# Optimization experiments

Measured on AMD Instinct MI355X. Metric: run time of the kernel, lower is better.

Reference implementation:

```python
import jax, jax.numpy as jnp
import numpy as np

B, NX, NY, C, H = 4, 1024, 1024, 768, 12
D = C // H  # head dim = 64
LN_EPS = 1e-5


def _dwconv(x_bcn, w, b, pad):
    # depthwise 1D conv: x [B,C,N], w [C,1,K], groups=C
    out = jax.lax.conv_general_dilated(
        x_bcn, w, window_strides=(1,), padding=[(pad, pad)],
        dimension_numbers=("NCH", "OIH", "NCH"), feature_group_count=C)
    return out + b[None, :, None]


def setup_inputs() -> dict:
    key = jax.random.key(0)
    ks = jax.random.split(key, 16)
    s = 0.02
    inp = {
        "x": jax.random.normal(ks[0], (B, NX, C), jnp.float32),
        "y": jax.random.normal(ks[1], (B, NY, C), jnp.float32),
        "conv1_w": jax.random.normal(ks[2], (C, 1, 3), jnp.float32) * s,
        "conv1_b": jnp.zeros((C,), jnp.float32),
        "conv2_w": jax.random.normal(ks[3], (C, 1, 5), jnp.float32) * s,
        "conv2_b": jnp.zeros((C,), jnp.float32),
        "conv3_w": jax.random.normal(ks[4], (C, 1, 7), jnp.float32) * s,
        "conv3_b": jnp.zeros((C,), jnp.float32),
        "ln_w": jnp.ones((C,), jnp.float32),
        "ln_b": jnp.zeros((C,), jnp.float32),
        "q_w": jax.random.normal(ks[5], (C, C), jnp.float32) * s,
        "kv_w": jax.random.normal(ks[6], (2 * C, C), jnp.float32) * s,
        "proj_w": jax.random.normal(ks[7], (C, C), jnp.float32) * s,
        "proj_b": jnp.zeros((C,), jnp.float32),
        "k1": int(NY * (1.0 / (1.0 + np.exp(-0.5)))),   # 637, from sigmoid(k_ratio1=0.5)
        "k2": int(NY * (1.0 / (1.0 + np.exp(-0.25)))),  # 575, from sigmoid(k_ratio2=0.25)
    }
    return inp


def reference(x, y, conv1_w, conv1_b, conv2_w, conv2_b, conv3_w, conv3_b,
              ln_w, ln_b, q_w, kv_w, proj_w, proj_b, k1, k2):
    yp = jnp.swapaxes(y, 1, 2)  # [B,C,Ny]
    # multi-scale depthwise convs; stride=1, same-padding -> all outputs length Ny,
    # so the original F.interpolate(size=target_len) is an exact identity.
    y_sum = _dwconv(yp, conv1_w, conv1_b, 1) + _dwconv(yp, conv2_w, conv2_b, 2) \
          + _dwconv(yp, conv3_w, conv3_b, 3)
    y_sum = jnp.swapaxes(y_sum, 1, 2)  # [B,Ny,C]
    # LayerNorm
    mu = y_sum.mean(-1, keepdims=True)
    var = ((y_sum - mu) ** 2).mean(-1, keepdims=True)
    y_norm = (y_sum - mu) * jax.lax.rsqrt(var + LN_EPS) * ln_w + ln_b
    # kv projection -> k,v [B,H,Ny,D]
    kv = (y_norm @ kv_w.T).reshape(B, NY, 2, H, D).transpose(2, 0, 3, 1, 4)
    k, v = kv[0], kv[1]
    q = (x @ q_w.T).reshape(B, NX, H, D).transpose(0, 2, 1, 3)  # [B,H,Nx,D]
    scale = D ** -0.5
    attn = jnp.einsum("bhqd,bhkd->bhqk", q, k) * scale  # [B,H,Nx,Ny]

    def topk_softmax(a, kk):
        # keep top-kk scores per row, mask rest to -inf, softmax
        kth = jax.lax.top_k(a, kk)[0][..., -1:]
        a_masked = jnp.where(a >= kth, a, -jnp.inf)
        return jax.nn.softmax(a_masked, axis=-1)

    out1 = jnp.einsum("bhqk,bhkd->bhqd", topk_softmax(attn, k1), v)
    out2 = jnp.einsum("bhqk,bhkd->bhqd", topk_softmax(attn, k2), v)
    out = 0.6 * out1 + 0.4 * out2
    out = out.transpose(0, 2, 1, 3).reshape(B, NX, C)
    out = out @ proj_w.T + proj_b
    return out + x
```

## Files before the change

### kernel.cpp

```cpp
#include <hip/hip_runtime.h>
#include <stdint.h>

#define B_ 4
#define NX_ 1024
#define NY_ 1024
#define C_ 768
#define H_ 12

using bf16x8 = __attribute__((ext_vector_type(8))) short;
using f32x4  = __attribute__((ext_vector_type(4))) float;

__device__ __forceinline__ unsigned short f2bf(float f) {
  union { float f; uint32_t u; } v; v.f = f;
  return (unsigned short)((v.u + 0x7FFFu + ((v.u >> 16) & 1u)) >> 16);
}
__device__ __forceinline__ float bf2f(uint32_t h) {
  union { uint32_t u; float f; } v; v.u = h << 16;
  return v.f;
}
__device__ __forceinline__ uint32_t umaxu(uint32_t a, uint32_t b) { return a > b ? a : b; }
__device__ __forceinline__ uint32_t uminu(uint32_t a, uint32_t b) { return a < b ? a : b; }
__device__ __forceinline__ uint32_t rfl(uint32_t v) {
  return (uint32_t)__builtin_amdgcn_readfirstlane((int)v);
}
__device__ __forceinline__ uint32_t key2h(uint32_t k) {
  return k ^ ((k & 0x8000u) ? 0x8000u : 0xFFFFu);
}
__device__ __forceinline__ float key2f(uint32_t k) { return bf2f(key2h(k)); }
__device__ __forceinline__ uint32_t f2key(float f) {
  const uint32_t h = f2bf(f);
  return h ^ (0x8000u | (0xFFFFu * (h >> 15)));
}

__global__ __launch_bounds__(256) void pre_kernel(
    const float* __restrict__ y,
    const float* __restrict__ w1, const float* __restrict__ b1,
    const float* __restrict__ w2, const float* __restrict__ b2,
    const float* __restrict__ w3, const float* __restrict__ b3,
    const float* __restrict__ lnw, const float* __restrict__ lnb,
    unsigned short* __restrict__ ynorm,
    const float4* __restrict__ x, uint2* __restrict__ xo,
    const float4* __restrict__ qw, uint2* __restrict__ qo,
    const float4* __restrict__ kvw, uint2* __restrict__ kvo,
    const float4* __restrict__ pw, uint2* __restrict__ po) {
  __shared__ float red[4][8];
  const int bid = blockIdx.x;
  const int t = threadIdx.x;
  if (bid >= 1024) {
    const int cid = bid - 1024;
    const float4* s; uint2* d; int base; float sc = 1.0f;
    if (cid < 3072)      { s = x;   d = xo;  base = cid;        sc = 0.125f * 1.44269504f; }
    else if (cid < 3648) { s = qw;  d = qo;  base = cid - 3072; }
    else if (cid < 4800) { s = kvw; d = kvo; base = cid - 3648; }
    else                 { s = pw;  d = po;  base = cid - 4800; }
    const int i = base * 256 + t;
    float4 v = s[i];
    uint2 p;
    p.x = (uint32_t)f2bf(v.x * sc) | ((uint32_t)f2bf(v.y * sc) << 16);
    p.y = (uint32_t)f2bf(v.z * sc) | ((uint32_t)f2bf(v.w * sc) << 16);
    d[i] = p;
    return;
  }
  const int b = bid >> 8, n0 = (bid & 255) << 2;
  const float* yb = y + (size_t)b * NY_ * C_;
  float v[3][4];
  #pragma unroll
  for (int ci = 0; ci < 3; ci++) {
    const int c = t + (ci << 8);
    float co[7];
    #pragma unroll
    for (int k = 0; k < 7; k++) co[k] = w3[c * 7 + k];
    #pragma unroll
    for (int k = 0; k < 5; k++) co[k + 1] += w2[c * 5 + k];
    #pragma unroll
    for (int k = 0; k < 3; k++) co[k + 2] += w1[c * 3 + k];
    const float bias = b1[c] + b2[c] + b3[c];
    float rv[10];
    #pragma unroll
    for (int rr = 0; rr < 10; rr++) {
      const int nn = n0 - 3 + rr;
      rv[rr] = (nn >= 0 && nn < NY_) ? yb[(size_t)nn * C_ + c] : 0.0f;
    }
    #pragma unroll
    for (int oi = 0; oi < 4; oi++) {
      float acc = bias;
      #pragma unroll
      for (int k = 0; k < 7; k++) acc = fmaf(co[k], rv[oi + k], acc);
      v[ci][oi] = acc;
    }
  }
  float s4[4], q4[4];
  #pragma unroll
  for (int oi = 0; oi < 4; oi++) {
    s4[oi] = v[0][oi] + v[1][oi] + v[2][oi];
    q4[oi] = v[0][oi] * v[0][oi] + v[1][oi] * v[1][oi] + v[2][oi] * v[2][oi];
  }
  #pragma unroll
  for (int m = 32; m >= 1; m >>= 1) {
    #pragma unroll
    for (int oi = 0; oi < 4; oi++) {
      s4[oi] += __shfl_xor(s4[oi], m);
      q4[oi] += __shfl_xor(q4[oi], m);
    }
  }
  const int wid = t >> 6;
  if ((t & 63) == 0) {
    #pragma unroll
    for (int oi = 0; oi < 4; oi++) { red[wid][oi] = s4[oi]; red[wid][4 + oi] = q4[oi]; }
  }
  __syncthreads();
  const float inv = 1.0f / 768.0f;
  #pragma unroll
  for (int oi = 0; oi < 4; oi++) {
    const float ts = red[0][oi] + red[1][oi] + red[2][oi] + red[3][oi];
    const float tq = red[0][4 + oi] + red[1][4 + oi] + red[2][4 + oi] + red[3][4 + oi];
    const float mu = ts * inv;
    const float var = tq * inv - mu * mu;
    const float rs = rsqrtf(var + 1e-5f);
    unsigned short* op = ynorm + (size_t)(b * 1024 + n0 + oi) * C_;
    #pragma unroll
    for (int ci = 0; ci < 3; ci++) {
      const int c = t + (ci << 8);
      op[c] = f2bf((v[ci][oi] - mu) * rs * lnw[c] + lnb[c]);
    }
  }
}

template <int ROWS>
__device__ __forceinline__ void stage_tile(const unsigned short* __restrict__ src,
                                           unsigned short* lds, int tid) {
  #pragma unroll
  for (int c = 0; c < ROWS / 32; c++) {
    const int lin = c * 4096 + (tid >> 6) * 1024 + (tid & 63) * 16;
    const int r = lin >> 7;
    const int koff = (lin & 127) ^ ((r & 7) << 4);
    const char* g = (const char*)(src + (size_t)r * 768) + koff;
    __builtin_amdgcn_global_load_lds(
        (const __attribute__((address_space(1))) uint32_t*)g,
        (__attribute__((address_space(3))) uint32_t*)(lds + (c * 2048 + (tid >> 6) * 512)),
        16, 0, 0);
  }
}

__device__ __forceinline__ void gemm_core(const unsigned short* __restrict__ A,
                                          const unsigned short* __restrict__ BT,
                                          int m0, int n0,
                                          unsigned short* Alds, unsigned short* Blds,
                                          f32x4 (&acc)[4][2]) {
  const int tid = threadIdx.x;
  const int l = tid & 63, w = tid >> 6;
  const int lr = l & 15, lk = l >> 4;
  const int wm = (w >> 1) * 64, wn = (w & 1) * 32;
  #pragma unroll
  for (int i = 0; i < 4; i++)
    #pragma unroll
    for (int j = 0; j < 2; j++) acc[i][j] = (f32x4){0.f, 0.f, 0.f, 0.f};

  for (int kt = 0; kt < 768; kt += 64) {
    __syncthreads();
    stage_tile<128>(A + (size_t)m0 * 768 + kt, Alds, tid);
    stage_tile<64>(BT + (size_t)n0 * 768 + kt, Blds, tid);
    asm volatile("s_waitcnt vmcnt(0)" ::: "memory");
    __syncthreads();
    #pragma unroll
    for (int s = 0; s < 2; s++) {
      bf16x8 a[4], b[2];
      #pragma unroll
      for (int i = 0; i < 4; i++) {
        const int r = wm + i * 16 + lr;
        const int byte = r * 128 + ((s * 64 + lk * 16) ^ ((r & 7) << 4));
        a[i] = *(const bf16x8*)((const char*)Alds + byte);
      }
      #pragma unroll
      for (int j = 0; j < 2; j++) {
        const int r = wn + j * 16 + lr;
        const int byte = r * 128 + ((s * 64 + lk * 16) ^ ((r & 7) << 4));
        b[j] = *(const bf16x8*)((const char*)Blds + byte);
      }
      #pragma unroll
      for (int i = 0; i < 4; i++)
        #pragma unroll
        for (int j = 0; j < 2; j++)
          acc[i][j] = __builtin_amdgcn_mfma_f32_16x16x32_bf16(a[i], b[j], acc[i][j], 0, 0, 0);
    }
  }
}

__global__ __launch_bounds__(256) void gemm_qkv_kernel(
    const unsigned short* __restrict__ xbf, const unsigned short* __restrict__ ynorm,
    const unsigned short* __restrict__ qwbf, const unsigned short* __restrict__ kvwbf,
    unsigned short* __restrict__ qbuf, unsigned short* __restrict__ kbuf,
    unsigned short* __restrict__ vtbuf) {
  __shared__ unsigned short Alds[128 * 64];
  __shared__ unsigned short Blds[64 * 64];
  const int bx = blockIdx.x;
  const bool isQ = bx < 12;
  const unsigned short* A = isQ ? xbf : ynorm;
  const unsigned short* BT = isQ ? qwbf : kvwbf;
  const int n0 = (isQ ? bx : bx - 12) * 64;
  const int m0 = blockIdx.y * 128;
  f32x4 acc[4][2];
  gemm_core(A, BT, m0, n0, Alds, Blds, acc);

  const int l = threadIdx.x & 63, w = threadIdx.x >> 6;
  const int lr = l & 15, lk = l >> 4;
  const int wm = (w >> 1) * 64, wn = (w & 1) * 32;
  #pragma unroll
  for (int i = 0; i < 4; i++) {
    const int r0 = m0 + wm + i * 16 + lk * 4;
    #pragma unroll
    for (int j = 0; j < 2; j++) {
      const int c = n0 + wn + j * 16 + lr;
      if (isQ) {
        const int h = c >> 6, d = c & 63;
        #pragma unroll
        for (int g = 0; g < 4; g++) {
          const int row = r0 + g;
          const int bb = row >> 10, nn = row & 1023;
          qbuf[((((size_t)bb * H_ + h) << 10) + nn) * 64 + d] = f2bf(acc[i][j][g]);
        }
      } else if (c < C_) {
        const int h = c >> 6, d = c & 63;
        #pragma unroll
        for (int g = 0; g < 4; g++) {
          const int row = r0 + g;
          const int bb = row >> 10, nn = row & 1023;
          kbuf[((((size_t)bb * H_ + h) << 10) + nn) * 64 + d] = f2bf(acc[i][j][g]);
        }
      } else {
        const int c2 = c - C_;
        const int h = c2 >> 6, d = c2 & 63;
        const int bb = r0 >> 10, nn = r0 & 1023;
        uint2 p;
        p.x = (uint32_t)f2bf(acc[i][j][0]) | ((uint32_t)f2bf(acc[i][j][1]) << 16);
        p.y = (uint32_t)f2bf(acc[i][j][2]) | ((uint32_t)f2bf(acc[i][j][3]) << 16);
        *(uint2*)(vtbuf + (((size_t)bb * H_ + h) * 64 + d) * 1024 + nn) = p;
      }
    }
  }
}

__global__ __launch_bounds__(256) void gemm_proj_kernel(
    const unsigned short* __restrict__ A, const unsigned short* __restrict__ BT,
    float* __restrict__ out, const float* __restrict__ bias,
    const float* __restrict__ resid) {
  __shared__ unsigned short Alds[128 * 64];
  __shared__ unsigned short Blds[64 * 64];
  const int n0 = blockIdx.x * 64;
  const int m0 = blockIdx.y * 128;
  f32x4 acc[4][2];
  gemm_core(A, BT, m0, n0, Alds, Blds, acc);

  const int l = threadIdx.x & 63, w = threadIdx.x >> 6;
  const int lr = l & 15, lk = l >> 4;
  const int wm = (w >> 1) * 64, wn = (w & 1) * 32;
  #pragma unroll
  for (int i = 0; i < 4; i++) {
    const int r0 = m0 + wm + i * 16 + lk * 4;
    #pragma unroll
    for (int j = 0; j < 2; j++) {
      const int c = n0 + wn + j * 16 + lr;
      #pragma unroll
      for (int g = 0; g < 4; g++) {
        const size_t idx = (size_t)(r0 + g) * C_ + c;
        out[idx] = acc[i][j][g] + bias[c] + resid[idx];
      }
    }
  }
}

struct SR { uint32_t t; uint32_t c; };
__device__ __forceinline__ SR searchk(const uint32_t (&k)[16], uint32_t kn,
                                      uint32_t lo, uint32_t clo, float flo,
                                      uint32_t hi, float fhi) {
  uint32_t chi = 0;
  #pragma unroll 1
  for (int it = 0; it < 16; ++it) {
    const int active = (clo > kn + 8u) && (lo + 1u < hi);
    if (!__builtin_amdgcn_readfirstlane(active)) break;
    uint32_t tk;
    if (it & 1) {
      tk = (lo + hi) >> 1;
    } else {
      const float tf = flo + (fhi - flo) * (float)(clo - kn) / (float)(clo - chi);
      tk = f2key(tf);
    }
    tk = uminu(umaxu(tk, lo + 1u), hi - 1u);
    uint32_t cnt = 0;
    #pragma unroll
    for (int i = 0; i < 16; i++) cnt += (k[i] >= tk) ? 1u : 0u;
    #pragma unroll
    for (int m = 32; m >= 1; m >>= 1) cnt += (uint32_t)__shfl_xor((int)cnt, m);
    const float tfk = key2f(tk);
    if (cnt >= kn) { lo = tk; clo = cnt; flo = tfk; }
    else           { hi = tk; chi = cnt; fhi = tfk; }
  }
  return {lo, clo};
}

__global__ __launch_bounds__(512, 8) void attn_kernel(
    const unsigned short* __restrict__ qbuf,
    const unsigned short* __restrict__ kbuf,
    const unsigned short* __restrict__ vtbuf,
    unsigned short* __restrict__ ao,
    const int* __restrict__ k1p, const int* __restrict__ k2p) {
  __shared__ unsigned short W[16 * 1024];
  __shared__ float P[16 * 66];
  const int l = threadIdx.x & 63, w = threadIdx.x >> 6;
  const int lr = l & 15, lk = l >> 4;
  const int bh = blockIdx.y, qt = blockIdx.x;
  const uint32_t kn1 = rfl(k1p[0]), kn2 = rfl(k2p[0]);
  const size_t base = (size_t)bh * NY_ * 64;
  const unsigned short* Q = qbuf + base + (size_t)qt * 16 * 64;
  const unsigned short* Kp = kbuf + base;
  const unsigned short* Vt = vtbuf + base;

  bf16x8 qf[2];
  #pragma unroll
  for (int s = 0; s < 2; s++)
    qf[s] = *(const bf16x8*)(Q + lr * 64 + s * 32 + lk * 8);

  #pragma unroll
  for (int kc = 0; kc < 2; kc++) {
    const int kbase = w * 128 + kc * 64;
    f32x4 acc[4];
    #pragma unroll
    for (int i = 0; i < 4; i++) acc[i] = (f32x4){0.f, 0.f, 0.f, 0.f};
    #pragma unroll
    for (int s = 0; s < 2; s++) {
      bf16x8 kf[4];
      #pragma unroll
      for (int i = 0; i < 4; i++)
        kf[i] = *(const bf16x8*)(Kp + (size_t)(kbase + i * 16 + lr) * 64 + s * 32 + lk * 8);
      #pragma unroll
      for (int i = 0; i < 4; i++)
        acc[i] = __builtin_amdgcn_mfma_f32_16x16x32_bf16(kf[i], qf[s], acc[i], 0, 0, 0);
    }
    #pragma unroll
    for (int i = 0; i < 4; i++) {
      const int kk = kbase + i * 16 + lk * 4;
      uint2 p;
      p.x = (uint32_t)f2bf(acc[i][0]) | ((uint32_t)f2bf(acc[i][1]) << 16);
      p.y = (uint32_t)f2bf(acc[i][2]) | ((uint32_t)f2bf(acc[i][3]) << 16);
      const int byte = lr * 2048 + ((kk * 2) ^ ((lr & 7) << 4));
      *(uint2*)((char*)W + byte) = p;
    }
  }
  __syncthreads();

  #pragma unroll 1
  for (int rr = 0; rr < 2; rr++) {
    char* rp = (char*)W + (2 * w + rr) * 2048;
    const uint4 u0 = *(uint4*)(rp + 16 * l);
    const uint4 u1 = *(uint4*)(rp + 16 * l + 1024);
    uint32_t k[16];
    {
      const uint32_t uu[8] = {u0.x, u0.y, u0.z, u0.w, u1.x, u1.y, u1.z, u1.w};
      #pragma unroll
      for (int i = 0; i < 8; i++) {
        const uint32_t h0 = uu[i] & 0xFFFFu, h1 = uu[i] >> 16;
        k[2 * i]     = h0 ^ (0x8000u | (0xFFFFu * (h0 >> 15)));
        k[2 * i + 1] = h1 ^ (0x8000u | (0xFFFFu * (h1 >> 15)));
      }
    }
    uint32_t kmx = 0;
    #pragma unroll
    for (int i = 0; i < 16; i++) kmx = umaxu(kmx, k[i]);
    #pragma unroll
    for (int m = 32; m >= 1; m >>= 1)
      kmx = umaxu(kmx, (uint32_t)__shfl_xor((int)kmx, m));
    const float fmx = key2f(kmx);

    const SR r1 = searchk(k, kn1, 0u, 1024u, fmx - 12.0f, kmx + 1u, fmx);
    const SR r2 = searchk(k, kn2, r1.t, r1.c, key2f(r1.t), kmx + 1u, fmx);
    const uint32_t t1 = r1.t, t2 = r2.t;

    float top = 0.f, band = 0.f;
    #pragma unroll
    for (int i = 0; i < 16; i++) {
      const float e = exp2f(key2f(k[i]) - fmx);
      if (k[i] >= t2) top += e;
      else if (k[i] >= t1) band += e;
    }
    #pragma unroll
    for (int m = 32; m >= 1; m >>= 1) {
      top += __shfl_xor(top, m);
      band += __shfl_xor(band, m);
    }
    const float c1 = 0.6f / (top + band), c2 = 0.4f / top;
    const float c12 = c1 + c2;
    uint32_t o[8];
    #pragma unroll
    for (int i = 0; i < 8; i++) {
      const int i0 = 2 * i, i1 = 2 * i + 1;
      const float cf0 = (k[i0] >= t1) ? ((k[i0] >= t2) ? c12 : c1) : 0.f;
      const float cf1 = (k[i1] >= t1) ? ((k[i1] >= t2) ? c12 : c1) : 0.f;
      const float w0 = exp2f(key2f(k[i0]) - fmx) * cf0;
      const float w1 = exp2f(key2f(k[i1]) - fmx) * cf1;
      o[i] = (uint32_t)f2bf(w0) | ((uint32_t)f2bf(w1) << 16);
    }
    *(uint4*)(rp + 16 * l)        = (uint4){o[0], o[1], o[2], o[3]};
    *(uint4*)(rp + 16 * l + 1024) = (uint4){o[4], o[5], o[6], o[7]};
  }
  __syncthreads();

  const int d0 = (w & 3) * 16;
  const int k0 = (w >> 2) * 512;
  f32x4 oacc = (f32x4){0.f, 0.f, 0.f, 0.f};
  #pragma unroll 4
  for (int kt2 = 0; kt2 < 512; kt2 += 32) {
    const int kt = k0 + kt2;
    const bf16x8 vf = *(const bf16x8*)(Vt + (size_t)(d0 + lr) * 1024 + kt + lk * 8);
    const int byte = lr * 2048 + (((kt + lk * 8) * 2) ^ ((lr & 7) << 4));
    const bf16x8 wf = *(const bf16x8*)((char*)W + byte);
    oacc = __builtin_amdgcn_mfma_f32_16x16x32_bf16(wf, vf, oacc, 0, 0, 0);
  }
  if (w >= 4) {
    #pragma unroll
    for (int g = 0; g < 4; g++)
      P[(lk * 4 + g) * 66 + d0 + lr] = oacc[g];
  }
  __syncthreads();
  if (w < 4) {
    const int b = bh / H_, h = bh % H_;
    #pragma unroll
    for (int g = 0; g < 4; g++) {
      const float v = oacc[g] + P[(lk * 4 + g) * 66 + d0 + lr];
      const int qrow = qt * 16 + lk * 4 + g;
      ao[(size_t)(b * NX_ + qrow) * C_ + h * 64 + d0 + lr] = f2bf(v);
    }
  }
}

extern "C" void kernel_launch(void* const* d_in, const int* in_sizes, int n_in,
                              void* d_out, int out_size, void* d_ws, size_t ws_size,
                              hipStream_t stream) {
  const float* x   = (const float*)d_in[0];
  const float* y   = (const float*)d_in[1];
  const float* w1  = (const float*)d_in[2];
  const float* b1  = (const float*)d_in[3];
  const float* w2  = (const float*)d_in[4];
  const float* b2  = (const float*)d_in[5];
  const float* w3  = (const float*)d_in[6];
  const float* b3  = (const float*)d_in[7];
  const float* lnw = (const float*)d_in[8];
  const float* lnb = (const float*)d_in[9];
  const float* qw  = (const float*)d_in[10];
  const float* kvw = (const float*)d_in[11];
  const float* pw  = (const float*)d_in[12];
  const float* pb  = (const float*)d_in[13];
  const int* k1p   = (const int*)d_in[14];
  const int* k2p   = (const int*)d_in[15];

  char* ws = (char*)d_ws;
  size_t off = 0;
  auto alloc = [&](size_t bytes) {
    char* p = ws + off;
    off += (bytes + 255) & ~(size_t)255;
    return p;
  };
  const size_t NTOK = (size_t)B_ * NX_ * C_;
  unsigned short* x_bf   = (unsigned short*)alloc(NTOK * 2);
  unsigned short* ynorm  = (unsigned short*)alloc(NTOK * 2);
  unsigned short* qw_bf  = (unsigned short*)alloc((size_t)C_ * C_ * 2);
  unsigned short* kvw_bf = (unsigned short*)alloc((size_t)2 * C_ * C_ * 2);
  unsigned short* pw_bf  = (unsigned short*)alloc((size_t)C_ * C_ * 2);
  unsigned short* qbuf   = (unsigned short*)alloc(NTOK * 2);
  unsigned short* kbuf   = (unsigned short*)alloc(NTOK * 2);
  unsigned short* vtbuf  = (unsigned short*)alloc(NTOK * 2);
  unsigned short* aobuf  = (unsigned short*)alloc(NTOK * 2);

  pre_kernel<<<6400, 256, 0, stream>>>(
      y, w1, b1, w2, b2, w3, b3, lnw, lnb, ynorm,
      (const float4*)x, (uint2*)x_bf, (const float4*)qw, (uint2*)qw_bf,
      (const float4*)kvw, (uint2*)kvw_bf, (const float4*)pw, (uint2*)pw_bf);

  gemm_qkv_kernel<<<dim3(36, 32), 256, 0, stream>>>(
      x_bf, ynorm, qw_bf, kvw_bf, qbuf, kbuf, vtbuf);

  attn_kernel<<<dim3(NX_ / 16, B_ * H_), 512, 0, stream>>>(qbuf, kbuf, vtbuf, aobuf, k1p, k2p);

  gemm_proj_kernel<<<dim3(12, 32), 256, 0, stream>>>(
      aobuf, pw_bf, (float*)d_out, pb, x);
}
```

Before: 295.1 us.

## Widen GEMM tiles to 128x128 and switch top-k threshold search to float domain

The GEMM core now computes 128x128 output tiles per block, with each wave owning a 64x64 sub-tile, instead of 128x64. This halves the grid for the QKV and projection GEMMs and improves operand reuse per LDS stage, at the cost of more accumulator registers and fewer blocks in flight. The attention top-k threshold search now runs on float scores rather than order-preserving integer keys. It starts from a Gaussian quantile guess built from the row mean and variance, alternates interpolation with bisection, and stops once the bracket is narrower than 1e-3. The attention kernel's occupancy hint drops from 8 to 6, and the early exit could let the chosen threshold differ slightly from the exact k-th value.

```diff
diff --git a/kernel.cpp b/kernel.cpp
--- a/kernel.cpp
+++ b/kernel.cpp
@@ -14,22 +14,8 @@
   union { float f; uint32_t u; } v; v.f = f;
   return (unsigned short)((v.u + 0x7FFFu + ((v.u >> 16) & 1u)) >> 16);
 }
-__device__ __forceinline__ float bf2f(uint32_t h) {
-  union { uint32_t u; float f; } v; v.u = h << 16;
-  return v.f;
-}
-__device__ __forceinline__ uint32_t umaxu(uint32_t a, uint32_t b) { return a > b ? a : b; }
-__device__ __forceinline__ uint32_t uminu(uint32_t a, uint32_t b) { return a < b ? a : b; }
 __device__ __forceinline__ uint32_t rfl(uint32_t v) {
   return (uint32_t)__builtin_amdgcn_readfirstlane((int)v);
-}
-__device__ __forceinline__ uint32_t key2h(uint32_t k) {
-  return k ^ ((k & 0x8000u) ? 0x8000u : 0xFFFFu);
-}
-__device__ __forceinline__ float key2f(uint32_t k) { return bf2f(key2h(k)); }
-__device__ __forceinline__ uint32_t f2key(float f) {
-  const uint32_t h = f2bf(f);
-  return h ^ (0x8000u | (0xFFFFu * (h >> 15)));
 }
 
 __global__ __launch_bounds__(256) void pre_kernel(
@@ -142,45 +128,45 @@
   }
 }
 
-__device__ __forceinline__ void gemm_core(const unsigned short* __restrict__ A,
-                                          const unsigned short* __restrict__ BT,
-                                          int m0, int n0,
-                                          unsigned short* Alds, unsigned short* Blds,
-                                          f32x4 (&acc)[4][2]) {
+__device__ __forceinline__ void gemm_core128(const unsigned short* __restrict__ A,
+                                             const unsigned short* __restrict__ BT,
+                                             int m0, int n0,
+                                             unsigned short* Alds, unsigned short* Blds,
+                                             f32x4 (&acc)[4][4]) {
   const int tid = threadIdx.x;
   const int l = tid & 63, w = tid >> 6;
   const int lr = l & 15, lk = l >> 4;
-  const int wm = (w >> 1) * 64, wn = (w & 1) * 32;
+  const int wr = (w >> 1) * 64, wc = (w & 1) * 64;
   #pragma unroll
   for (int i = 0; i < 4; i++)
     #pragma unroll
-    for (int j = 0; j < 2; j++) acc[i][j] = (f32x4){0.f, 0.f, 0.f, 0.f};
+    for (int j = 0; j < 4; j++) acc[i][j] = (f32x4){0.f, 0.f, 0.f, 0.f};
 
   for (int kt = 0; kt < 768; kt += 64) {
     __syncthreads();
     stage_tile<128>(A + (size_t)m0 * 768 + kt, Alds, tid);
-    stage_tile<64>(BT + (size_t)n0 * 768 + kt, Blds, tid);
+    stage_tile<128>(BT + (size_t)n0 * 768 + kt, Blds, tid);
     asm volatile("s_waitcnt vmcnt(0)" ::: "memory");
     __syncthreads();
     #pragma unroll
     for (int s = 0; s < 2; s++) {
-      bf16x8 a[4], b[2];
+      bf16x8 a[4], b[4];
       #pragma unroll
       for (int i = 0; i < 4; i++) {
-        const int r = wm + i * 16 + lr;
+        const int r = wr + i * 16 + lr;
         const int byte = r * 128 + ((s * 64 + lk * 16) ^ ((r & 7) << 4));
         a[i] = *(const bf16x8*)((const char*)Alds + byte);
       }
       #pragma unroll
-      for (int j = 0; j < 2; j++) {
-        const int r = wn + j * 16 + lr;
+      for (int j = 0; j < 4; j++) {
+        const int r = wc + j * 16 + lr;
         const int byte = r * 128 + ((s * 64 + lk * 16) ^ ((r & 7) << 4));
         b[j] = *(const bf16x8*)((const char*)Blds + byte);
       }
       #pragma unroll
       for (int i = 0; i < 4; i++)
         #pragma unroll
-        for (int j = 0; j < 2; j++)
+        for (int j = 0; j < 4; j++)
           acc[i][j] = __builtin_amdgcn_mfma_f32_16x16x32_bf16(a[i], b[j], acc[i][j], 0, 0, 0);
     }
   }
@@ -192,25 +178,25 @@
     unsigned short* __restrict__ qbuf, unsigned short* __restrict__ kbuf,
     unsigned short* __restrict__ vtbuf) {
   __shared__ unsigned short Alds[128 * 64];
-  __shared__ unsigned short Blds[64 * 64];
+  __shared__ unsigned short Blds[128 * 64];
   const int bx = blockIdx.x;
-  const bool isQ = bx < 12;
+  const bool isQ = bx < 6;
   const unsigned short* A = isQ ? xbf : ynorm;
   const unsigned short* BT = isQ ? qwbf : kvwbf;
-  const int n0 = (isQ ? bx : bx - 12) * 64;
+  const int n0 = (isQ ? bx : bx - 6) * 128;
   const int m0 = blockIdx.y * 128;
-  f32x4 acc[4][2];
-  gemm_core(A, BT, m0, n0, Alds, Blds, acc);
+  f32x4 acc[4][4];
+  gemm_core128(A, BT, m0, n0, Alds, Blds, acc);
 
   const int l = threadIdx.x & 63, w = threadIdx.x >> 6;
   const int lr = l & 15, lk = l >> 4;
-  const int wm = (w >> 1) * 64, wn = (w & 1) * 32;
+  const int wr = (w >> 1) * 64, wc = (w & 1) * 64;
   #pragma unroll
   for (int i = 0; i < 4; i++) {
-    const int r0 = m0 + wm + i * 16 + lk * 4;
-    #pragma unroll
-    for (int j = 0; j < 2; j++) {
-      const int c = n0 + wn + j * 16 + lr;
+    const int r0 = m0 + wr + i * 16 + lk * 4;
+    #pragma unroll
+    for (int j = 0; j < 4; j++) {
+      const int c = n0 + wc + j * 16 + lr;
       if (isQ) {
         const int h = c >> 6, d = c & 63;
         #pragma unroll
@@ -245,21 +231,21 @@
     float* __restrict__ out, const float* __restrict__ bias,
     const float* __restrict__ resid) {
   __shared__ unsigned short Alds[128 * 64];
-  __shared__ unsigned short Blds[64 * 64];
-  const int n0 = blockIdx.x * 64;
+  __shared__ unsigned short Blds[128 * 64];
+  const int n0 = blockIdx.x * 128;
   const int m0 = blockIdx.y * 128;
-  f32x4 acc[4][2];
-  gemm_core(A, BT, m0, n0, Alds, Blds, acc);
+  f32x4 acc[4][4];
+  gemm_core128(A, BT, m0, n0, Alds, Blds, acc);
 
   const int l = threadIdx.x & 63, w = threadIdx.x >> 6;
   const int lr = l & 15, lk = l >> 4;
-  const int wm = (w >> 1) * 64, wn = (w & 1) * 32;
+  const int wr = (w >> 1) * 64, wc = (w & 1) * 64;
   #pragma unroll
   for (int i = 0; i < 4; i++) {
-    const int r0 = m0 + wm + i * 16 + lk * 4;
-    #pragma unroll
-    for (int j = 0; j < 2; j++) {
-      const int c = n0 + wn + j * 16 + lr;
+    const int r0 = m0 + wr + i * 16 + lk * 4;
+    #pragma unroll
+    for (int j = 0; j < 4; j++) {
+      const int c = n0 + wc + j * 16 + lr;
       #pragma unroll
       for (int g = 0; g < 4; g++) {
         const size_t idx = (size_t)(r0 + g) * C_ + c;
@@ -269,36 +255,31 @@
   }
 }
 
-struct SR { uint32_t t; uint32_t c; };
-__device__ __forceinline__ SR searchk(const uint32_t (&k)[16], uint32_t kn,
-                                      uint32_t lo, uint32_t clo, float flo,
-                                      uint32_t hi, float fhi) {
-  uint32_t chi = 0;
+struct SRf { float t; uint32_t c; };
+__device__ __forceinline__ SRf searchf(const float (&s)[16], uint32_t kn,
+                                       float flo, uint32_t clo,
+                                       float fhi, uint32_t chi, float guess) {
+  float tf = guess;
   #pragma unroll 1
-  for (int it = 0; it < 16; ++it) {
-    const int active = (clo > kn + 8u) && (lo + 1u < hi);
-    if (!__builtin_amdgcn_readfirstlane(active)) break;
-    uint32_t tk;
-    if (it & 1) {
-      tk = (lo + hi) >> 1;
-    } else {
-      const float tf = flo + (fhi - flo) * (float)(clo - kn) / (float)(clo - chi);
-      tk = f2key(tf);
-    }
-    tk = uminu(umaxu(tk, lo + 1u), hi - 1u);
+  for (int it = 0; it < 12; ++it) {
+    if (!__builtin_amdgcn_readfirstlane((int)(clo > kn + 8u))) break;
+    if (!(tf > flo && tf < fhi)) tf = 0.5f * (flo + fhi);
     uint32_t cnt = 0;
     #pragma unroll
-    for (int i = 0; i < 16; i++) cnt += (k[i] >= tk) ? 1u : 0u;
+    for (int i = 0; i < 16; i++) cnt += (s[i] >= tf) ? 1u : 0u;
     #pragma unroll
     for (int m = 32; m >= 1; m >>= 1) cnt += (uint32_t)__shfl_xor((int)cnt, m);
-    const float tfk = key2f(tk);
-    if (cnt >= kn) { lo = tk; clo = cnt; flo = tfk; }
-    else           { hi = tk; chi = cnt; fhi = tfk; }
-  }
-  return {lo, clo};
-}
-
-__global__ __launch_bounds__(512, 8) void attn_kernel(
+    if (cnt >= kn) { flo = tf; clo = cnt; }
+    else           { fhi = tf; chi = cnt; }
+    if (fhi - flo < 1e-3f) break;
+    tf = (it & 1) ? 0.5f * (flo + fhi)
+                  : flo + (fhi - flo) * (float)(int)(clo - kn) /
+                        fmaxf((float)(int)(clo - chi), 1.0f);
+  }
+  return {flo, clo};
+}
+
+__global__ __launch_bounds__(512, 6) void attn_kernel(
     const unsigned short* __restrict__ qbuf,
     const unsigned short* __restrict__ kbuf,
     const unsigned short* __restrict__ vtbuf,
@@ -353,50 +334,59 @@
     char* rp = (char*)W + (2 * w + rr) * 2048;
     const uint4 u0 = *(uint4*)(rp + 16 * l);
     const uint4 u1 = *(uint4*)(rp + 16 * l + 1024);
-    uint32_t k[16];
+    float s[16];
     {
       const uint32_t uu[8] = {u0.x, u0.y, u0.z, u0.w, u1.x, u1.y, u1.z, u1.w};
       #pragma unroll
       for (int i = 0; i < 8; i++) {
-        const uint32_t h0 = uu[i] & 0xFFFFu, h1 = uu[i] >> 16;
-        k[2 * i]     = h0 ^ (0x8000u | (0xFFFFu * (h0 >> 15)));
-        k[2 * i + 1] = h1 ^ (0x8000u | (0xFFFFu * (h1 >> 15)));
+        s[2 * i]     = __uint_as_float(uu[i] << 16);
+        s[2 * i + 1] = __uint_as_float(uu[i] & 0xFFFF0000u);
       }
     }
-    uint32_t kmx = 0;
-    #pragma unroll
-    for (int i = 0; i < 16; i++) kmx = umaxu(kmx, k[i]);
-    #pragma unroll
-    for (int m = 32; m >= 1; m >>= 1)
-      kmx = umaxu(kmx, (uint32_t)__shfl_xor((int)kmx, m));
-    const float fmx = key2f(kmx);
-
-    const SR r1 = searchk(k, kn1, 0u, 1024u, fmx - 12.0f, kmx + 1u, fmx);
-    const SR r2 = searchk(k, kn2, r1.t, r1.c, key2f(r1.t), kmx + 1u, fmx);
-    const uint32_t t1 = r1.t, t2 = r2.t;
-
-    float top = 0.f, band = 0.f;
+    float mx = s[0], sm = 0.f, sq = 0.f;
     #pragma unroll
     for (int i = 0; i < 16; i++) {
-      const float e = exp2f(key2f(k[i]) - fmx);
-      if (k[i] >= t2) top += e;
-      else if (k[i] >= t1) band += e;
+      mx = fmaxf(mx, s[i]);
+      sm += s[i];
+      sq = fmaf(s[i], s[i], sq);
     }
     #pragma unroll
     for (int m = 32; m >= 1; m >>= 1) {
-      top += __shfl_xor(top, m);
-      band += __shfl_xor(band, m);
-    }
-    const float c1 = 0.6f / (top + band), c2 = 0.4f / top;
-    const float c12 = c1 + c2;
+      mx = fmaxf(mx, __shfl_xor(mx, m));
+      sm += __shfl_xor(sm, m);
+      sq += __shfl_xor(sq, m);
+    }
+    const float mu = sm * (1.f / 1024.f);
+    const float sg = sqrtf(fmaxf(sq * (1.f / 1024.f) - mu * mu, 0.f));
+    const float z1 = (0.5f - (float)kn1 * (1.f / 1024.f)) * 2.5066f;
+    const float z2 = (0.5f - (float)kn2 * (1.f / 1024.f)) * 2.5066f;
+    const SRf r1 = searchf(s, kn1, mx - 130.f, 1024u, mx + 1.f, 0u, mu + z1 * sg);
+    const SRf r2 = searchf(s, kn2, r1.t, r1.c, mx + 1.f, 0u, fmaxf(mu + z2 * sg, r1.t));
+    const float t1 = r1.t, t2 = r2.t;
+
+    float e[16], s1 = 0.f, s2 = 0.f;
+    #pragma unroll
+    for (int i = 0; i < 16; i++) {
+      const float ev = exp2f(s[i] - mx);
+      e[i] = ev;
+      if (s[i] >= t1) s1 += ev;
+      if (s[i] >= t2) s2 += ev;
+    }
+    const float et1 = exp2f(t1 - mx), et2 = exp2f(t2 - mx);
+    #pragma unroll
+    for (int m = 32; m >= 1; m >>= 1) {
+      s1 += __shfl_xor(s1, m);
+      s2 += __shfl_xor(s2, m);
+    }
+    const float c1 = 0.6f / fmaxf(s1, 1e-20f);
+    const float c2v = 0.4f / fmaxf(s2, 1e-20f);
+    const float c12 = c1 + c2v;
     uint32_t o[8];
     #pragma unroll
     for (int i = 0; i < 8; i++) {
-      const int i0 = 2 * i, i1 = 2 * i + 1;
-      const float cf0 = (k[i0] >= t1) ? ((k[i0] >= t2) ? c12 : c1) : 0.f;
-      const float cf1 = (k[i1] >= t1) ? ((k[i1] >= t2) ? c12 : c1) : 0.f;
-      const float w0 = exp2f(key2f(k[i0]) - fmx) * cf0;
-      const float w1 = exp2f(key2f(k[i1]) - fmx) * cf1;
+      const float e0 = e[2 * i], e1 = e[2 * i + 1];
+      const float w0 = e0 * ((e0 >= et1) ? ((e0 >= et2) ? c12 : c1) : 0.f);
+      const float w1 = e1 * ((e1 >= et1) ? ((e1 >= et2) ? c12 : c1) : 0.f);
       o[i] = (uint32_t)f2bf(w0) | ((uint32_t)f2bf(w1) << 16);
     }
     *(uint4*)(rp + 16 * l)        = (uint4){o[0], o[1], o[2], o[3]};
@@ -475,11 +465,11 @@
       (const float4*)x, (uint2*)x_bf, (const float4*)qw, (uint2*)qw_bf,
       (const float4*)kvw, (uint2*)kvw_bf, (const float4*)pw, (uint2*)pw_bf);
 
-  gemm_qkv_kernel<<<dim3(36, 32), 256, 0, stream>>>(
+  gemm_qkv_kernel<<<dim3(18, 32), 256, 0, stream>>>(
       x_bf, ynorm, qw_bf, kvw_bf, qbuf, kbuf, vtbuf);
 
   attn_kernel<<<dim3(NX_ / 16, B_ * H_), 512, 0, stream>>>(qbuf, kbuf, vtbuf, aobuf, k1p, k2p);
 
-  gemm_proj_kernel<<<dim3(12, 32), 256, 0, stream>>>(
+  gemm_proj_kernel<<<dim3(6, 32), 256, 0, stream>>>(
       aobuf, pw_bf, (float*)d_out, pb, x);
 }
```

Result: faster. 270.2 us (-8.4%).
